# Kernel optimization log

Hardware: AMD Instinct MI355X
Metric: run time of the kernel (lower is better)

Reference implementation:

```python
import jax, jax.numpy as jnp
import numpy as np

R, E, A, F, K = 1024, 512, 128, 32, 31  # rnn_dim, embed_dim, attn_dim, n_filters, kernel
B, T = 64, 2048


def setup_inputs() -> dict:
    key = jax.random.key(0)
    ks = jax.random.split(key, 10)
    return {
        "attention_hidden": jax.random.normal(ks[0], (B, R), jnp.float32),
        "memory": jax.random.normal(ks[1], (B, T, E), jnp.float32),
        "attention_weights_cat": jax.random.uniform(ks[2], (B, 2, T), jnp.float32),
        "mask": jax.random.randint(ks[3], (B, T), 0, 2, jnp.int32),
        "W_query": jax.random.normal(ks[4], (R, A), jnp.float32) / np.sqrt(R),
        "W_memory": jax.random.normal(ks[5], (E, A), jnp.float32) / np.sqrt(E),
        "conv_w": jax.random.normal(ks[6], (F, 2, K), jnp.float32) / np.sqrt(2 * K),  # OIH
        "W_loc": jax.random.normal(ks[7], (F, A), jnp.float32) / np.sqrt(F),
        "v_w": jax.random.normal(ks[8], (A,), jnp.float32) / np.sqrt(A),
        "v_b": jax.random.normal(ks[9], (1,), jnp.float32) * 0.0,
    }


def reference(attention_hidden, memory, attention_weights_cat, mask,
              W_query, W_memory, conv_w, W_loc, v_w, v_b):
    # processed query: (B, A)
    pq = attention_hidden @ W_query
    # processed memory: (B, T, A)
    pm = jnp.einsum('bte,ea->bta', memory, W_memory)
    # location features: conv1d over (B, 2, T) with 'same' padding, no bias
    loc = jax.lax.conv_general_dilated(
        attention_weights_cat, conv_w,
        window_strides=(1,), padding=[((K - 1) // 2, (K - 1) // 2)],
        dimension_numbers=('NCH', 'OIH', 'NCH'))  # (B, F, T)
    pl = jnp.einsum('bft,fa->bta', loc, W_loc)  # (B, T, A)
    # energies: v(tanh(pm + pq + pl)) -> (B, T)
    energies = jnp.tanh(pm + pq[:, None, :] + pl) @ v_w + v_b[0]
    alignments = energies + mask.astype(energies.dtype) * -1e25
    attention_weights = jax.nn.softmax(alignments, axis=-1)
    # NOTE: original code (faithfully) uses raw alignments, not softmax weights
    attention_output = jnp.einsum('bt,bte->be', alignments, memory)
    return attention_output, attention_weights
```

## Files before the change

### kernel.cpp

```cpp
#include <hip/hip_runtime.h>

#define Bsz 64
#define Tsz 2048
#define Esz 512
#define Asz 128
#define Rsz 1024
#define KP  576
#define TILE_M 64

typedef __bf16 bf16;
typedef __bf16 bf16x8 __attribute__((ext_vector_type(8)));
typedef __bf16 bf16x4 __attribute__((ext_vector_type(4)));
typedef float  f32x4  __attribute__((ext_vector_type(4)));

__global__ __launch_bounds__(128) void prep_kernel(
    const float* __restrict__ Wmem, const float* __restrict__ convw,
    const float* __restrict__ Wloc, const float* __restrict__ ah,
    const float* __restrict__ Wq, bf16* __restrict__ Wext,
    float* __restrict__ pq)
{
  int blk = blockIdx.x, tid = threadIdx.x;
  if (blk < Asz) {
    int a = blk;
    for (int e = tid; e < Esz; e += 128)
      Wext[a*KP + e] = (bf16)Wmem[e*Asz + a];
    if (tid < 64) {
      int j = tid;
      float u = 0.f;
      if (j < 62) {
        int c  = (j < 31) ? 0 : 1;
        int kk = (j < 31) ? j : j - 31;
        #pragma unroll
        for (int f = 0; f < 32; ++f)
          u += convw[f*62 + c*31 + kk] * Wloc[f*Asz + a];
      }
      Wext[a*KP + Esz + j] = (bf16)u;
    }
  } else {
    int b = blk - Asz;
    int a = tid;
    float s = 0.f;
    for (int r = 0; r < Rsz; ++r)
      s += ah[b*Rsz + r] * Wq[r*Asz + a];
    pq[b*Asz + a] = s;
  }
}

__global__ __launch_bounds__(256) void attn_main(
    const float* __restrict__ memory, const float* __restrict__ awcat,
    const int* __restrict__ mask, const bf16* __restrict__ Wext,
    const float* __restrict__ pq, const float* __restrict__ vw,
    const float* __restrict__ vb, float* __restrict__ out,
    float* __restrict__ ws_align)
{
  __shared__ bf16  Afull[TILE_M * KP];
  __shared__ float s_pq[Asz];
  __shared__ float s_vw[Asz];
  __shared__ float s_ebuf[TILE_M];
  __shared__ float s_align[TILE_M];

  int tid = threadIdx.x;
  int b  = blockIdx.x >> 5;
  int t0 = (blockIdx.x & 31) << 6;

  const float4* memv = (const float4*)(memory + (size_t)(b*Tsz + t0)*Esz);
  for (int i = tid; i < TILE_M*(Esz/4); i += 256) {
    int r = i >> 7, c4 = i & 127;
    float4 v = memv[r*128 + c4];
    int k = c4 * 4;
    int sw = (k >> 3) ^ (r & 7);
    int base = r*KP + sw*8 + (k & 7);
    bf16x4 p; p[0]=(bf16)v.x; p[1]=(bf16)v.y; p[2]=(bf16)v.z; p[3]=(bf16)v.w;
    *(bf16x4*)&Afull[base] = p;
  }
  const float* aw = awcat + (size_t)b*2*Tsz;
  for (int i = tid; i < TILE_M*64; i += 256) {
    int r = i >> 6, j = i & 63;
    float val = 0.f;
    if (j < 62) {
      int c  = (j < 31) ? 0 : 1;
      int kk = (j < 31) ? j : j - 31;
      int t  = t0 + r + kk - 15;
      if (t >= 0 && t < Tsz) val = aw[c*Tsz + t];
    }
    int k = Esz + j;
    int sw = (k >> 3) ^ (r & 7);
    Afull[r*KP + sw*8 + (k & 7)] = (bf16)val;
  }
  if (tid < Asz) { s_pq[tid] = pq[b*Asz + tid]; s_vw[tid] = vw[tid]; }
  if (tid < TILE_M) s_ebuf[tid] = 0.f;
  __syncthreads();

  int w = tid >> 6, l = tid & 63;
  int quad = l >> 4, lrow = l & 15;

  f32x4 acc[4][2];
  #pragma unroll
  for (int mt = 0; mt < 4; ++mt)
    #pragma unroll
    for (int nt = 0; nt < 2; ++nt)
      acc[mt][nt] = (f32x4){0.f, 0.f, 0.f, 0.f};

  for (int kc = 0; kc < KP/32; ++kc) {
    int kbase = kc*32 + quad*8;
    bf16x8 bfrag[2];
    #pragma unroll
    for (int nt = 0; nt < 2; ++nt) {
      int acol = lrow + 16*(2*w + nt);
      bfrag[nt] = *(const bf16x8*)&Wext[acol*KP + kbase];
    }
    bf16x8 afrag[4];
    #pragma unroll
    for (int mt = 0; mt < 4; ++mt) {
      int r = mt*16 + lrow;
      int sw = ((kbase >> 3) ^ (r & 7));
      afrag[mt] = *(const bf16x8*)&Afull[r*KP + sw*8];
    }
    #pragma unroll
    for (int mt = 0; mt < 4; ++mt)
      #pragma unroll
      for (int nt = 0; nt < 2; ++nt)
        acc[mt][nt] = __builtin_amdgcn_mfma_f32_16x16x32_bf16(
            afrag[mt], bfrag[nt], acc[mt][nt], 0, 0, 0);
  }

  float partial[4][4];
  #pragma unroll
  for (int mt = 0; mt < 4; ++mt)
    #pragma unroll
    for (int rg = 0; rg < 4; ++rg) partial[mt][rg] = 0.f;
  #pragma unroll
  for (int nt = 0; nt < 2; ++nt) {
    int col = 16*(2*w + nt) + lrow;
    float vwc = s_vw[col], pqc = s_pq[col];
    #pragma unroll
    for (int mt = 0; mt < 4; ++mt)
      #pragma unroll
      for (int rg = 0; rg < 4; ++rg)
        partial[mt][rg] += tanhf(acc[mt][nt][rg] + pqc) * vwc;
  }
  #pragma unroll
  for (int off = 1; off < 16; off <<= 1)
    #pragma unroll
    for (int mt = 0; mt < 4; ++mt)
      #pragma unroll
      for (int rg = 0; rg < 4; ++rg)
        partial[mt][rg] += __shfl_xor(partial[mt][rg], off, 64);
  if (lrow == 0) {
    #pragma unroll
    for (int mt = 0; mt < 4; ++mt)
      #pragma unroll
      for (int rg = 0; rg < 4; ++rg)
        atomicAdd(&s_ebuf[mt*16 + quad*4 + rg], partial[mt][rg]);
  }
  __syncthreads();

  if (tid < TILE_M) {
    int t = t0 + tid;
    float al = s_ebuf[tid] + vb[0] + (float)mask[b*Tsz + t] * -1e25f;
    s_align[tid] = al;
    ws_align[b*Tsz + t] = al;
  }
  __syncthreads();

  float a0 = 0.f, a1 = 0.f;
  int k0 = tid, k1 = tid + 256;
  for (int r = 0; r < TILE_M; ++r) {
    float al = s_align[r];
    float m0 = (float)Afull[r*KP + (((k0 >> 3) ^ (r & 7)) << 3) + (k0 & 7)];
    float m1 = (float)Afull[r*KP + (((k1 >> 3) ^ (r & 7)) << 3) + (k1 & 7)];
    a0 += al * m0;
    a1 += al * m1;
  }
  atomicAdd(&out[b*Esz + k0], a0);
  atomicAdd(&out[b*Esz + k1], a1);
}

__global__ __launch_bounds__(256) void softmax_kernel(
    const float* __restrict__ ws_align, float* __restrict__ out_w)
{
  int b = blockIdx.x, tid = threadIdx.x;
  const float* row = ws_align + (size_t)b*Tsz;
  float vals[8];
  float lmax = -3.4e38f;
  #pragma unroll
  for (int i = 0; i < 8; ++i) { vals[i] = row[tid + i*256]; lmax = fmaxf(lmax, vals[i]); }
  #pragma unroll
  for (int off = 1; off < 64; off <<= 1) lmax = fmaxf(lmax, __shfl_xor(lmax, off, 64));
  __shared__ float smax[4], ssum[4];
  if ((tid & 63) == 0) smax[tid >> 6] = lmax;
  __syncthreads();
  float bmax = fmaxf(fmaxf(smax[0], smax[1]), fmaxf(smax[2], smax[3]));
  float lsum = 0.f;
  #pragma unroll
  for (int i = 0; i < 8; ++i) { vals[i] = __expf(vals[i] - bmax); lsum += vals[i]; }
  #pragma unroll
  for (int off = 1; off < 64; off <<= 1) lsum += __shfl_xor(lsum, off, 64);
  if ((tid & 63) == 0) ssum[tid >> 6] = lsum;
  __syncthreads();
  float inv = 1.f / (ssum[0] + ssum[1] + ssum[2] + ssum[3]);
  #pragma unroll
  for (int i = 0; i < 8; ++i) out_w[(size_t)b*Tsz + tid + i*256] = vals[i] * inv;
}

extern "C" void kernel_launch(void* const* d_in, const int* in_sizes, int n_in,
                              void* d_out, int out_size, void* d_ws, size_t ws_size,
                              hipStream_t stream) {
  const float* ah   = (const float*)d_in[0];
  const float* mem  = (const float*)d_in[1];
  const float* awc  = (const float*)d_in[2];
  const int*   mask = (const int*)d_in[3];
  const float* Wq   = (const float*)d_in[4];
  const float* Wm   = (const float*)d_in[5];
  const float* cw   = (const float*)d_in[6];
  const float* Wl   = (const float*)d_in[7];
  const float* vw   = (const float*)d_in[8];
  const float* vb   = (const float*)d_in[9];
  float* out = (float*)d_out;

  bf16*  Wext = (bf16*)d_ws;
  float* pq   = (float*)((char*)d_ws + 147456);
  float* wsa  = (float*)((char*)d_ws + 180224);

  hipMemsetAsync(out, 0, Bsz*Esz*sizeof(float), stream);
  prep_kernel<<<dim3(Asz + Bsz), 128, 0, stream>>>(Wm, cw, Wl, ah, Wq, Wext, pq);
  attn_main<<<dim3(Bsz*(Tsz/TILE_M)), 256, 0, stream>>>(mem, awc, mask, Wext, pq, vw, vb, out, wsa);
  softmax_kernel<<<dim3(Bsz), 256, 0, stream>>>(wsa, out + Bsz*Esz);
}
```

Baseline: 515.4 us.

## Halve attention tile, split prep work across more blocks, vectorize pq and context loops

The main kernel tile shrinks from 64 to 32 time steps, doubling the block count and halving LDS use per block so more blocks can be resident. The prep kernel moves to 256 threads, gives the conv-weight fold its own blocks, and computes pq with float4 loads and a K-split reduced through shared memory. The context accumulation reads two adjacent bf16 values per thread. In exchange, the smaller tile doubles the global atomic adds into the output and reloads the Wext fragments twice as often.

```diff
diff --git a/kernel.cpp b/kernel.cpp
--- a/kernel.cpp
+++ b/kernel.cpp
@@ -6,43 +6,59 @@
 #define Asz 128
 #define Rsz 1024
 #define KP  576
-#define TILE_M 64
+#define TILE_M 32
 
 typedef __bf16 bf16;
 typedef __bf16 bf16x8 __attribute__((ext_vector_type(8)));
 typedef __bf16 bf16x4 __attribute__((ext_vector_type(4)));
+typedef __bf16 bf16x2 __attribute__((ext_vector_type(2)));
 typedef float  f32x4  __attribute__((ext_vector_type(4)));
 
-__global__ __launch_bounds__(128) void prep_kernel(
+__global__ __launch_bounds__(256) void prep_kernel(
     const float* __restrict__ Wmem, const float* __restrict__ convw,
     const float* __restrict__ Wloc, const float* __restrict__ ah,
     const float* __restrict__ Wq, bf16* __restrict__ Wext,
     float* __restrict__ pq)
 {
+  __shared__ f32x4 red[256];
   int blk = blockIdx.x, tid = threadIdx.x;
-  if (blk < Asz) {
+  if (blk < 128) {
     int a = blk;
-    for (int e = tid; e < Esz; e += 128)
+    #pragma unroll
+    for (int e = tid; e < Esz; e += 256)
       Wext[a*KP + e] = (bf16)Wmem[e*Asz + a];
-    if (tid < 64) {
-      int j = tid;
-      float u = 0.f;
-      if (j < 62) {
-        int c  = (j < 31) ? 0 : 1;
-        int kk = (j < 31) ? j : j - 31;
-        #pragma unroll
-        for (int f = 0; f < 32; ++f)
-          u += convw[f*62 + c*31 + kk] * Wloc[f*Asz + a];
-      }
-      Wext[a*KP + Esz + j] = (bf16)u;
-    }
+  } else if (blk < 160) {
+    int idx = (blk - 128)*256 + tid;
+    int a = idx >> 6, j = idx & 63;
+    float u = 0.f;
+    if (j < 62) {
+      int c  = (j < 31) ? 0 : 1;
+      int kk = (j < 31) ? j : j - 31;
+      #pragma unroll
+      for (int f = 0; f < 32; ++f)
+        u += convw[f*62 + c*31 + kk] * Wloc[f*Asz + a];
+    }
+    Wext[a*KP + Esz + j] = (bf16)u;
   } else {
-    int b = blk - Asz;
-    int a = tid;
-    float s = 0.f;
-    for (int r = 0; r < Rsz; ++r)
-      s += ah[b*Rsz + r] * Wq[r*Asz + a];
-    pq[b*Asz + a] = s;
+    int b  = blk - 160;
+    int cg = tid & 31;
+    int kg = tid >> 5;
+    const float* ahb = ah + (size_t)b*Rsz;
+    f32x4 s = (f32x4){0.f,0.f,0.f,0.f};
+    int r0 = kg*128;
+    for (int r = r0; r < r0 + 128; ++r) {
+      float av = ahb[r];
+      f32x4 wq = *(const f32x4*)&Wq[r*Asz + cg*4];
+      s += av * wq;
+    }
+    red[tid] = s;
+    __syncthreads();
+    if (tid < 32) {
+      f32x4 tot = red[tid];
+      #pragma unroll
+      for (int g = 1; g < 8; ++g) tot += red[g*32 + tid];
+      *(f32x4*)&pq[b*Asz + tid*4] = tot;
+    }
   }
 }
 
@@ -60,10 +76,11 @@
   __shared__ float s_align[TILE_M];
 
   int tid = threadIdx.x;
-  int b  = blockIdx.x >> 5;
-  int t0 = (blockIdx.x & 31) << 6;
+  int b  = blockIdx.x >> 6;
+  int t0 = (blockIdx.x & 63) << 5;
 
   const float4* memv = (const float4*)(memory + (size_t)(b*Tsz + t0)*Esz);
+  #pragma unroll
   for (int i = tid; i < TILE_M*(Esz/4); i += 256) {
     int r = i >> 7, c4 = i & 127;
     float4 v = memv[r*128 + c4];
@@ -74,6 +91,7 @@
     *(bf16x4*)&Afull[base] = p;
   }
   const float* aw = awcat + (size_t)b*2*Tsz;
+  #pragma unroll
   for (int i = tid; i < TILE_M*64; i += 256) {
     int r = i >> 6, j = i & 63;
     float val = 0.f;
@@ -94,9 +112,9 @@
   int w = tid >> 6, l = tid & 63;
   int quad = l >> 4, lrow = l & 15;
 
-  f32x4 acc[4][2];
-  #pragma unroll
-  for (int mt = 0; mt < 4; ++mt)
+  f32x4 acc[2][2];
+  #pragma unroll
+  for (int mt = 0; mt < 2; ++mt)
     #pragma unroll
     for (int nt = 0; nt < 2; ++nt)
       acc[mt][nt] = (f32x4){0.f, 0.f, 0.f, 0.f};
@@ -109,24 +127,24 @@
       int acol = lrow + 16*(2*w + nt);
       bfrag[nt] = *(const bf16x8*)&Wext[acol*KP + kbase];
     }
-    bf16x8 afrag[4];
-    #pragma unroll
-    for (int mt = 0; mt < 4; ++mt) {
+    bf16x8 afrag[2];
+    #pragma unroll
+    for (int mt = 0; mt < 2; ++mt) {
       int r = mt*16 + lrow;
       int sw = ((kbase >> 3) ^ (r & 7));
       afrag[mt] = *(const bf16x8*)&Afull[r*KP + sw*8];
     }
     #pragma unroll
-    for (int mt = 0; mt < 4; ++mt)
+    for (int mt = 0; mt < 2; ++mt)
       #pragma unroll
       for (int nt = 0; nt < 2; ++nt)
         acc[mt][nt] = __builtin_amdgcn_mfma_f32_16x16x32_bf16(
             afrag[mt], bfrag[nt], acc[mt][nt], 0, 0, 0);
   }
 
-  float partial[4][4];
-  #pragma unroll
-  for (int mt = 0; mt < 4; ++mt)
+  float partial[2][4];
+  #pragma unroll
+  for (int mt = 0; mt < 2; ++mt)
     #pragma unroll
     for (int rg = 0; rg < 4; ++rg) partial[mt][rg] = 0.f;
   #pragma unroll
@@ -134,7 +152,7 @@
     int col = 16*(2*w + nt) + lrow;
     float vwc = s_vw[col], pqc = s_pq[col];
     #pragma unroll
-    for (int mt = 0; mt < 4; ++mt)
+    for (int mt = 0; mt < 2; ++mt)
       #pragma unroll
       for (int rg = 0; rg < 4; ++rg)
         partial[mt][rg] += tanhf(acc[mt][nt][rg] + pqc) * vwc;
@@ -142,13 +160,13 @@
   #pragma unroll
   for (int off = 1; off < 16; off <<= 1)
     #pragma unroll
-    for (int mt = 0; mt < 4; ++mt)
+    for (int mt = 0; mt < 2; ++mt)
       #pragma unroll
       for (int rg = 0; rg < 4; ++rg)
         partial[mt][rg] += __shfl_xor(partial[mt][rg], off, 64);
   if (lrow == 0) {
     #pragma unroll
-    for (int mt = 0; mt < 4; ++mt)
+    for (int mt = 0; mt < 2; ++mt)
       #pragma unroll
       for (int rg = 0; rg < 4; ++rg)
         atomicAdd(&s_ebuf[mt*16 + quad*4 + rg], partial[mt][rg]);
@@ -163,17 +181,18 @@
   }
   __syncthreads();
 
+  int k0 = tid * 2;
   float a0 = 0.f, a1 = 0.f;
-  int k0 = tid, k1 = tid + 256;
+  #pragma unroll
   for (int r = 0; r < TILE_M; ++r) {
     float al = s_align[r];
-    float m0 = (float)Afull[r*KP + (((k0 >> 3) ^ (r & 7)) << 3) + (k0 & 7)];
-    float m1 = (float)Afull[r*KP + (((k1 >> 3) ^ (r & 7)) << 3) + (k1 & 7)];
-    a0 += al * m0;
-    a1 += al * m1;
-  }
-  atomicAdd(&out[b*Esz + k0], a0);
-  atomicAdd(&out[b*Esz + k1], a1);
+    int sw = ((k0 >> 3) ^ (r & 7));
+    bf16x2 m = *(const bf16x2*)&Afull[r*KP + sw*8 + (k0 & 7)];
+    a0 += al * (float)m[0];
+    a1 += al * (float)m[1];
+  }
+  atomicAdd(&out[b*Esz + k0],     a0);
+  atomicAdd(&out[b*Esz + k0 + 1], a1);
 }
 
 __global__ __launch_bounds__(256) void softmax_kernel(
@@ -223,7 +242,7 @@
   float* wsa  = (float*)((char*)d_ws + 180224);
 
   hipMemsetAsync(out, 0, Bsz*Esz*sizeof(float), stream);
-  prep_kernel<<<dim3(Asz + Bsz), 128, 0, stream>>>(Wm, cw, Wl, ah, Wq, Wext, pq);
+  prep_kernel<<<dim3(224), 256, 0, stream>>>(Wm, cw, Wl, ah, Wq, Wext, pq);
   attn_main<<<dim3(Bsz*(Tsz/TILE_M)), 256, 0, stream>>>(mem, awc, mask, Wext, pq, vw, vb, out, wsa);
   softmax_kernel<<<dim3(Bsz), 256, 0, stream>>>(wsa, out + Bsz*Esz);
 }
```

New measurement: 496.6 us. 1.04x faster.
